# Performance work log

Hardware: AMD Instinct MI355X
Metric: run time of the kernel (lower is better)

## Reference

```python
import jax, jax.numpy as jnp
import numpy as np

N_NODES = 50000
N_EDGES = 800000
HIDDEN = 128


def setup_inputs() -> dict:
    key = jax.random.key(0)
    k_h, k_src, k_dst, k_w1, k_w2 = jax.random.split(key, 5)
    h = jax.random.normal(k_h, (N_NODES, HIDDEN), dtype=jnp.float32)
    src = jax.random.randint(k_src, (N_EDGES,), 0, N_NODES, dtype=jnp.int32)
    dst = jax.random.randint(k_dst, (N_EDGES,), 0, N_NODES, dtype=jnp.int32)
    edge_index = jnp.stack([src, dst], axis=0)
    # MLP params (torch Linear: y = x @ W.T + b); store as [in, out] for einsum
    s1 = 1.0 / np.sqrt(2 * HIDDEN)
    s2 = 1.0 / np.sqrt(HIDDEN)
    W1 = jax.random.uniform(k_w1, (2 * HIDDEN, HIDDEN), jnp.float32, -s1, s1)
    b1 = jnp.zeros((HIDDEN,), jnp.float32)
    W2 = jax.random.uniform(k_w2, (HIDDEN, HIDDEN), jnp.float32, -s2, s2)
    b2 = jnp.zeros((HIDDEN,), jnp.float32)
    return {"h": h, "edge_index": edge_index, "W1": W1, "b1": b1, "W2": W2, "b2": b2}


def reference(h, edge_index, W1, b1, W2, b2):
    src, dst = edge_index[0], edge_index[1]
    n = h.shape[0]
    # scatter-add of gathered source features -> agg [N, H]
    agg = jax.ops.segment_sum(h[src], dst, num_segments=n)
    # degree normalization (clamp_min 1)
    deg = jax.ops.segment_sum(jnp.ones_like(dst, dtype=h.dtype), dst, num_segments=n)
    deg = jnp.maximum(deg, 1.0)[:, None]
    agg = agg / deg
    x = jnp.concatenate([h, agg], axis=1)  # [N, 2H]
    x = jax.nn.relu(x @ W1 + b1)
    x = jax.nn.relu(x @ W2 + b2)
    return x
```

## Files before the change

### kernel.cpp

```cpp
#include <hip/hip_runtime.h>

typedef unsigned short u16;
typedef unsigned int u32;
typedef __attribute__((ext_vector_type(8))) short short8;
typedef __attribute__((ext_vector_type(4))) float f32x4;
typedef __attribute__((ext_vector_type(4))) u32 u32x4;

#define BKT_SHIFT 6
#define BKT_NODES 64
#define CAP 1536
#define EPB 4096
#define NBH 1024

__device__ inline u16 f2bf(float f){ u32 u=__float_as_uint(f); u32 r=((u>>16)&1u)+0x7fffu; return (u16)((u+r)>>16); }

__global__ __launch_bounds__(256) void k_castbin(
    const int* __restrict__ src, const int* __restrict__ dst,
    int* __restrict__ gcnt, u32* __restrict__ recs_g, int nE, int gB,
    const float* __restrict__ h, u16* __restrict__ hbf, int nh8,
    const float* __restrict__ w1, const float* __restrict__ w2,
    u16* __restrict__ w1t, u16* __restrict__ w2t){
  __shared__ u32 rl[EPB];
  __shared__ int hist[NBH];
  __shared__ int curs[NBH];
  int t = threadIdx.x;
  if ((int)blockIdx.x < gB){
    int e0 = blockIdx.x*EPB;
    for (int i=t;i<NBH;i+=256) hist[i]=0;
    __syncthreads();
    #pragma unroll
    for (int i=0;i<EPB/256;i++){
      int e = e0 + i*256 + t;
      u32 rec = 0xffffffffu;
      if (e < nE){
        u32 d = (u32)dst[e];
        u32 s = (u32)src[e];
        u32 bb = d >> BKT_SHIFT;
        rec = (bb<<22) | ((d & (u32)(BKT_NODES-1))<<16) | s;
        atomicAdd(&hist[bb & (NBH-1)], 1);
      }
      rl[i*256+t] = rec;
    }
    __syncthreads();
    for (int i=t;i<NBH;i+=256){
      int c = hist[i];
      curs[i] = c ? atomicAdd(&gcnt[i], c) : 0;
    }
    __syncthreads();
    #pragma unroll
    for (int i=0;i<EPB/256;i++){
      u32 rec = rl[i*256+t];
      if (rec != 0xffffffffu){
        u32 bb = rec>>22;
        int slot = atomicAdd(&curs[bb], 1);
        if (slot < CAP) recs_g[(size_t)bb*CAP + slot] = rec & 0x3fffffu;
      }
    }
  } else {
    int e = ((int)blockIdx.x - gB)*256 + t;
    if (e < nh8){
      float4 a = *(const float4*)(h + (size_t)e*8);
      float4 b = *(const float4*)(h + (size_t)e*8 + 4);
      u32x4 p;
      p.x = (u32)f2bf(a.x) | ((u32)f2bf(a.y)<<16);
      p.y = (u32)f2bf(a.z) | ((u32)f2bf(a.w)<<16);
      p.z = (u32)f2bf(b.x) | ((u32)f2bf(b.y)<<16);
      p.w = (u32)f2bf(b.z) | ((u32)f2bf(b.w)<<16);
      *(u32x4*)(hbf + (size_t)e*8) = p;
    }
    if (e < 256*128){ int k=e>>7, nn=e&127; w1t[nn*256+k]=f2bf(w1[e]); }
    else { int j=e-256*128; if (j<128*128){ int k=j>>7, nn=j&127; w2t[nn*128+k]=f2bf(w2[j]); } }
  }
}

__global__ __launch_bounds__(256, 3) void k_aggmlp(
    const u16* __restrict__ hbf, const u32* __restrict__ recs_g,
    const int* __restrict__ gcnt,
    const u16* __restrict__ w1t, const u16* __restrict__ w2t,
    const float* __restrict__ b1, const float* __restrict__ b2,
    float* __restrict__ out, int n){
  __shared__ __align__(16) u16 xs[64*264];
  __shared__ u32 stage[CAP];
  __shared__ u16 srt[CAP];
  __shared__ int hist[BKT_NODES];
  __shared__ int scn[BKT_NODES];
  __shared__ int cur[BKT_NODES];
  int b = blockIdx.x, t = threadIdx.x;
  int node0 = b*BKT_NODES;

  #pragma unroll
  for (int i=0;i<8;i++){
    int idx = i*256 + t;
    int row = idx>>5, c8 = idx&31;
    int node = node0 + row;
    u32x4 v = {0,0,0,0};
    if (node < n && c8 < 16) v = *(const u32x4*)(hbf + (size_t)node*128 + c8*8);
    *(u32x4*)(&xs[row*264 + c8*8]) = v;
  }

  int cnt = gcnt[b]; if (cnt > CAP) cnt = CAP;
  if (t < BKT_NODES) hist[t] = 0;
  __syncthreads();
  for (int i=t; i<cnt; i+=256){
    u32 r = recs_g[(size_t)b*CAP + i];
    stage[i] = r;
    atomicAdd(&hist[(r>>16)&(BKT_NODES-1)], 1);
  }
  __syncthreads();
  if (t < BKT_NODES) scn[t] = hist[t];
  __syncthreads();
  #pragma unroll
  for (int d=1; d<BKT_NODES; d<<=1){
    int v = 0;
    if (t < BKT_NODES){ v = scn[t]; if (t >= d) v += scn[t-d]; }
    __syncthreads();
    if (t < BKT_NODES) scn[t] = v;
    __syncthreads();
  }
  if (t < BKT_NODES) cur[t] = scn[t] - hist[t];
  __syncthreads();
  for (int i=t; i<cnt; i+=256){
    u32 r = stage[i];
    int slot = atomicAdd(&cur[(r>>16)&(BKT_NODES-1)], 1);
    srt[slot] = (u16)(r & 0xffffu);
  }
  __syncthreads();

  int grp = t>>4, l16g = t&15;
  for (int i=0;i<4;i++){
    int nl = grp*4 + i;
    int node = node0 + nl;
    int deg = 0, st = 0;
    if (node < n){ deg = hist[nl]; st = scn[nl] - deg; }
    float a[8] = {0.f,0.f,0.f,0.f,0.f,0.f,0.f,0.f};
    for (int base=0; base<deg; base+=16){
      int sidx[16];
      #pragma unroll
      for (int j=0;j<16;j++){
        int jj = base + j; if (jj > deg-1) jj = deg-1;
        sidx[j] = srt[st + jj];
      }
      u32x4 vv[16];
      #pragma unroll
      for (int j=0;j<16;j++)
        vv[j] = *(const u32x4*)(hbf + (size_t)sidx[j]*128 + l16g*8);
      #pragma unroll
      for (int j=0;j<16;j++){
        float m = (base+j < deg) ? 1.f : 0.f;
        #pragma unroll
        for (int q=0;q<4;q++){
          u32 u = vv[j][q];
          union{u32 v; float f;} lo,hi; lo.v=u<<16; hi.v=u&0xffff0000u;
          a[q*2]   += m*lo.f;
          a[q*2+1] += m*hi.f;
        }
      }
    }
    if (node < n){
      float inv = 1.f/(float)(deg>0?deg:1);
      u32x4 o;
      o.x = (u32)f2bf(a[0]*inv) | ((u32)f2bf(a[1]*inv)<<16);
      o.y = (u32)f2bf(a[2]*inv) | ((u32)f2bf(a[3]*inv)<<16);
      o.z = (u32)f2bf(a[4]*inv) | ((u32)f2bf(a[5]*inv)<<16);
      o.w = (u32)f2bf(a[6]*inv) | ((u32)f2bf(a[7]*inv)<<16);
      *(u32x4*)(&xs[nl*264 + 128 + l16g*8]) = o;
    }
  }

  int wave=t>>6, lane=t&63, quad=lane>>4, l16=lane&15;
  int nt0 = wave*2;
  const u16* w1p0 = w1t + (size_t)((nt0  )*16 + l16)*256 + quad*8;
  const u16* w1p1 = w1t + (size_t)((nt0+1)*16 + l16)*256 + quad*8;
  short8 wb1[16];
  #pragma unroll
  for (int ks=0;ks<8;ks++){
    wb1[ks*2+0] = *(const short8*)(w1p0 + ks*32);
    wb1[ks*2+1] = *(const short8*)(w1p1 + ks*32);
  }
  __syncthreads();

  f32x4 acc[4][2];
  #pragma unroll
  for (int m=0;m<4;m++){ acc[m][0]=(f32x4){0,0,0,0}; acc[m][1]=(f32x4){0,0,0,0}; }
  #pragma unroll
  for (int ks=0;ks<8;ks++){
    #pragma unroll
    for (int m=0;m<4;m++){
      short8 av = *(const short8*)(&xs[(m*16+l16)*264 + ks*32 + quad*8]);
      acc[m][0] = __builtin_amdgcn_mfma_f32_16x16x32_bf16(av, wb1[ks*2+0], acc[m][0],0,0,0);
      acc[m][1] = __builtin_amdgcn_mfma_f32_16x16x32_bf16(av, wb1[ks*2+1], acc[m][1],0,0,0);
    }
  }

  const u16* w2p0 = w2t + (size_t)((nt0  )*16 + l16)*128 + quad*8;
  const u16* w2p1 = w2t + (size_t)((nt0+1)*16 + l16)*128 + quad*8;
  short8 wb2[8];
  #pragma unroll
  for (int ks=0;ks<4;ks++){
    wb2[ks*2+0] = *(const short8*)(w2p0 + ks*32);
    wb2[ks*2+1] = *(const short8*)(w2p1 + ks*32);
  }
  __syncthreads();

  float bias0 = b1[(nt0  )*16 + l16];
  float bias1 = b1[(nt0+1)*16 + l16];
  #pragma unroll
  for (int m=0;m<4;m++){
    #pragma unroll
    for (int r=0;r<4;r++){
      int row = m*16 + quad*4 + r;
      float v0 = acc[m][0][r] + bias0; v0 = v0>0.f ? v0 : 0.f;
      float v1 = acc[m][1][r] + bias1; v1 = v1>0.f ? v1 : 0.f;
      xs[row*264 + (nt0  )*16 + l16] = f2bf(v0);
      xs[row*264 + (nt0+1)*16 + l16] = f2bf(v1);
    }
  }
  __syncthreads();

  f32x4 acc2[4][2];
  #pragma unroll
  for (int m=0;m<4;m++){ acc2[m][0]=(f32x4){0,0,0,0}; acc2[m][1]=(f32x4){0,0,0,0}; }
  #pragma unroll
  for (int ks=0;ks<4;ks++){
    #pragma unroll
    for (int m=0;m<4;m++){
      short8 av = *(const short8*)(&xs[(m*16+l16)*264 + ks*32 + quad*8]);
      acc2[m][0] = __builtin_amdgcn_mfma_f32_16x16x32_bf16(av, wb2[ks*2+0], acc2[m][0],0,0,0);
      acc2[m][1] = __builtin_amdgcn_mfma_f32_16x16x32_bf16(av, wb2[ks*2+1], acc2[m][1],0,0,0);
    }
  }
  float c0 = b2[(nt0  )*16 + l16];
  float c1 = b2[(nt0+1)*16 + l16];
  #pragma unroll
  for (int m=0;m<4;m++){
    #pragma unroll
    for (int r=0;r<4;r++){
      int node = node0 + m*16 + quad*4 + r;
      if (node<n){
        float v0 = acc2[m][0][r]+c0; v0 = v0>0.f?v0:0.f;
        float v1 = acc2[m][1][r]+c1; v1 = v1>0.f?v1:0.f;
        out[(size_t)node*128 + (nt0  )*16 + l16] = v0;
        out[(size_t)node*128 + (nt0+1)*16 + l16] = v1;
      }
    }
  }
}

extern "C" void kernel_launch(void* const* d_in, const int* in_sizes, int n_in,
                              void* d_out, int out_size, void* d_ws, size_t ws_size,
                              hipStream_t stream){
  const float* h  = (const float*)d_in[0];
  const int*   ei = (const int*)d_in[1];
  const float* W1 = (const float*)d_in[2];
  const float* b1 = (const float*)d_in[3];
  const float* W2 = (const float*)d_in[4];
  const float* b2 = (const float*)d_in[5];
  float* out = (float*)d_out;
  int n  = in_sizes[0] / 128;
  int nE = in_sizes[1] / 2;
  const int* srcI = ei;
  const int* dstI = ei + nE;
  int nbuck = (n + BKT_NODES - 1) >> BKT_SHIFT;

  char* ws = (char*)d_ws;
  u32* recs = (u32*)ws;
  size_t off = (size_t)nbuck*CAP*4;
  int* gcnt = (int*)(ws + off); off += 4096;
  u16* hbf  = (u16*)(ws + off); off += (size_t)n*256;
  off = (off + 15) & ~(size_t)15;
  u16* w1t  = (u16*)(ws + off);
  u16* w2t  = (u16*)(ws + off + 65536);

  hipMemsetAsync(gcnt, 0, NBH*sizeof(int), stream);
  int gB = (nE + EPB - 1)/EPB;
  int nh8 = n*16;
  int castN = nh8 > 49152 ? nh8 : 49152;
  int gC = (castN + 255)/256;
  k_castbin<<<gB+gC, 256, 0, stream>>>(srcI, dstI, gcnt, recs, nE, gB,
                                       h, hbf, nh8, W1, W2, w1t, w2t);
  k_aggmlp<<<nbuck, 256, 0, stream>>>(hbf, recs, gcnt, w1t, w2t, b1, b2, out, n);
}
```

Before: 151.4 us.

## Double block size to 512 threads and split work across eight waves

The fused aggregate+MLP kernel now runs 512 threads per block. Each wave owns one 16-column output tile instead of two, and each 16-lane group aggregates two nodes with 8-edge batches instead of four nodes with 16-edge batches. The LDS stage buffer is dropped, so records are re-read from global memory, and the 64-entry prefix scan uses wave shuffles instead of barrier-separated LDS steps. This is meant to raise parallelism and memory-level concurrency in the gather while cutting barriers and register pressure. In exchange it loads the record list from global memory twice and lowers per-thread gather depth.

```diff
diff --git a/kernel.cpp b/kernel.cpp
--- a/kernel.cpp
+++ b/kernel.cpp
@@ -73,79 +73,74 @@
   }
 }
 
-__global__ __launch_bounds__(256, 3) void k_aggmlp(
+__global__ __launch_bounds__(512, 6) void k_aggmlp(
     const u16* __restrict__ hbf, const u32* __restrict__ recs_g,
     const int* __restrict__ gcnt,
     const u16* __restrict__ w1t, const u16* __restrict__ w2t,
     const float* __restrict__ b1, const float* __restrict__ b2,
     float* __restrict__ out, int n){
   __shared__ __align__(16) u16 xs[64*264];
-  __shared__ u32 stage[CAP];
   __shared__ u16 srt[CAP];
   __shared__ int hist[BKT_NODES];
   __shared__ int scn[BKT_NODES];
   __shared__ int cur[BKT_NODES];
   int b = blockIdx.x, t = threadIdx.x;
   int node0 = b*BKT_NODES;
-
-  #pragma unroll
-  for (int i=0;i<8;i++){
-    int idx = i*256 + t;
+  int cnt = gcnt[b]; if (cnt > CAP) cnt = CAP;
+  const u32* rp = recs_g + (size_t)b*CAP;
+
+  if (t < BKT_NODES) hist[t] = 0;
+  #pragma unroll
+  for (int i=0;i<4;i++){
+    int idx = i*512 + t;
     int row = idx>>5, c8 = idx&31;
     int node = node0 + row;
     u32x4 v = {0,0,0,0};
     if (node < n && c8 < 16) v = *(const u32x4*)(hbf + (size_t)node*128 + c8*8);
     *(u32x4*)(&xs[row*264 + c8*8]) = v;
   }
-
-  int cnt = gcnt[b]; if (cnt > CAP) cnt = CAP;
-  if (t < BKT_NODES) hist[t] = 0;
-  __syncthreads();
-  for (int i=t; i<cnt; i+=256){
-    u32 r = recs_g[(size_t)b*CAP + i];
-    stage[i] = r;
-    atomicAdd(&hist[(r>>16)&(BKT_NODES-1)], 1);
-  }
-  __syncthreads();
-  if (t < BKT_NODES) scn[t] = hist[t];
-  __syncthreads();
-  #pragma unroll
-  for (int d=1; d<BKT_NODES; d<<=1){
-    int v = 0;
-    if (t < BKT_NODES){ v = scn[t]; if (t >= d) v += scn[t-d]; }
-    __syncthreads();
-    if (t < BKT_NODES) scn[t] = v;
-    __syncthreads();
-  }
-  if (t < BKT_NODES) cur[t] = scn[t] - hist[t];
-  __syncthreads();
-  for (int i=t; i<cnt; i+=256){
-    u32 r = stage[i];
+  __syncthreads();
+  for (int i=t; i<cnt; i+=512) atomicAdd(&hist[(rp[i]>>16)&(BKT_NODES-1)], 1);
+  __syncthreads();
+  if (t < BKT_NODES){
+    int v = hist[t];
+    int s = v;
+    #pragma unroll
+    for (int d=1; d<64; d<<=1){
+      int o = __shfl_up(s, d, 64);
+      if (t >= d) s += o;
+    }
+    scn[t] = s;
+    cur[t] = s - v;
+  }
+  __syncthreads();
+  for (int i=t; i<cnt; i+=512){
+    u32 r = rp[i];
     int slot = atomicAdd(&cur[(r>>16)&(BKT_NODES-1)], 1);
     srt[slot] = (u16)(r & 0xffffu);
   }
   __syncthreads();
 
   int grp = t>>4, l16g = t&15;
-  for (int i=0;i<4;i++){
-    int nl = grp*4 + i;
-    int node = node0 + nl;
-    int deg = 0, st = 0;
-    if (node < n){ deg = hist[nl]; st = scn[nl] - deg; }
+  #pragma unroll
+  for (int i=0;i<2;i++){
+    int nl = i*32 + grp;
+    int deg = hist[nl];
+    int st  = scn[nl] - deg;
     float a[8] = {0.f,0.f,0.f,0.f,0.f,0.f,0.f,0.f};
-    for (int base=0; base<deg; base+=16){
-      int sidx[16];
+    for (int base=0; base<deg; base+=8){
+      int sidx[8];
       #pragma unroll
-      for (int j=0;j<16;j++){
+      for (int j=0;j<8;j++){
         int jj = base + j; if (jj > deg-1) jj = deg-1;
         sidx[j] = srt[st + jj];
       }
-      u32x4 vv[16];
+      u32x4 vv[8];
       #pragma unroll
-      for (int j=0;j<16;j++)
+      for (int j=0;j<8;j++)
         vv[j] = *(const u32x4*)(hbf + (size_t)sidx[j]*128 + l16g*8);
       #pragma unroll
-      for (int j=0;j<16;j++){
+      for (int j=0;j<8;j++){
         float m = (base+j < deg) ? 1.f : 0.f;
         #pragma unroll
         for (int q=0;q<4;q++){
@@ -156,91 +151,72 @@
         }
       }
     }
-    if (node < n){
-      float inv = 1.f/(float)(deg>0?deg:1);
-      u32x4 o;
-      o.x = (u32)f2bf(a[0]*inv) | ((u32)f2bf(a[1]*inv)<<16);
-      o.y = (u32)f2bf(a[2]*inv) | ((u32)f2bf(a[3]*inv)<<16);
-      o.z = (u32)f2bf(a[4]*inv) | ((u32)f2bf(a[5]*inv)<<16);
-      o.w = (u32)f2bf(a[6]*inv) | ((u32)f2bf(a[7]*inv)<<16);
-      *(u32x4*)(&xs[nl*264 + 128 + l16g*8]) = o;
-    }
+    float inv = 1.f/(float)(deg>0?deg:1);
+    u32x4 o;
+    o.x = (u32)f2bf(a[0]*inv) | ((u32)f2bf(a[1]*inv)<<16);
+    o.y = (u32)f2bf(a[2]*inv) | ((u32)f2bf(a[3]*inv)<<16);
+    o.z = (u32)f2bf(a[4]*inv) | ((u32)f2bf(a[5]*inv)<<16);
+    o.w = (u32)f2bf(a[6]*inv) | ((u32)f2bf(a[7]*inv)<<16);
+    *(u32x4*)(&xs[nl*264 + 128 + l16g*8]) = o;
   }
 
   int wave=t>>6, lane=t&63, quad=lane>>4, l16=lane&15;
-  int nt0 = wave*2;
-  const u16* w1p0 = w1t + (size_t)((nt0  )*16 + l16)*256 + quad*8;
-  const u16* w1p1 = w1t + (size_t)((nt0+1)*16 + l16)*256 + quad*8;
-  short8 wb1[16];
-  #pragma unroll
-  for (int ks=0;ks<8;ks++){
-    wb1[ks*2+0] = *(const short8*)(w1p0 + ks*32);
-    wb1[ks*2+1] = *(const short8*)(w1p1 + ks*32);
-  }
-  __syncthreads();
-
-  f32x4 acc[4][2];
-  #pragma unroll
-  for (int m=0;m<4;m++){ acc[m][0]=(f32x4){0,0,0,0}; acc[m][1]=(f32x4){0,0,0,0}; }
+  const u16* w1p = w1t + (size_t)(wave*16 + l16)*256 + quad*8;
+  short8 wb1[8];
+  #pragma unroll
+  for (int ks=0;ks<8;ks++) wb1[ks] = *(const short8*)(w1p + ks*32);
+  __syncthreads();
+
+  f32x4 acc[4];
+  #pragma unroll
+  for (int m=0;m<4;m++) acc[m]=(f32x4){0,0,0,0};
   #pragma unroll
   for (int ks=0;ks<8;ks++){
     #pragma unroll
     for (int m=0;m<4;m++){
       short8 av = *(const short8*)(&xs[(m*16+l16)*264 + ks*32 + quad*8]);
-      acc[m][0] = __builtin_amdgcn_mfma_f32_16x16x32_bf16(av, wb1[ks*2+0], acc[m][0],0,0,0);
-      acc[m][1] = __builtin_amdgcn_mfma_f32_16x16x32_bf16(av, wb1[ks*2+1], acc[m][1],0,0,0);
-    }
-  }
-
-  const u16* w2p0 = w2t + (size_t)((nt0  )*16 + l16)*128 + quad*8;
-  const u16* w2p1 = w2t + (size_t)((nt0+1)*16 + l16)*128 + quad*8;
-  short8 wb2[8];
-  #pragma unroll
-  for (int ks=0;ks<4;ks++){
-    wb2[ks*2+0] = *(const short8*)(w2p0 + ks*32);
-    wb2[ks*2+1] = *(const short8*)(w2p1 + ks*32);
-  }
-  __syncthreads();
-
-  float bias0 = b1[(nt0  )*16 + l16];
-  float bias1 = b1[(nt0+1)*16 + l16];
+      acc[m] = __builtin_amdgcn_mfma_f32_16x16x32_bf16(av, wb1[ks], acc[m],0,0,0);
+    }
+  }
+
+  const u16* w2p = w2t + (size_t)(wave*16 + l16)*128 + quad*8;
+  short8 wb2[4];
+  #pragma unroll
+  for (int ks=0;ks<4;ks++) wb2[ks] = *(const short8*)(w2p + ks*32);
+  __syncthreads();
+
+  float bias = b1[wave*16 + l16];
   #pragma unroll
   for (int m=0;m<4;m++){
     #pragma unroll
     for (int r=0;r<4;r++){
       int row = m*16 + quad*4 + r;
-      float v0 = acc[m][0][r] + bias0; v0 = v0>0.f ? v0 : 0.f;
-      float v1 = acc[m][1][r] + bias1; v1 = v1>0.f ? v1 : 0.f;
-      xs[row*264 + (nt0  )*16 + l16] = f2bf(v0);
-      xs[row*264 + (nt0+1)*16 + l16] = f2bf(v1);
-    }
-  }
-  __syncthreads();
-
-  f32x4 acc2[4][2];
-  #pragma unroll
-  for (int m=0;m<4;m++){ acc2[m][0]=(f32x4){0,0,0,0}; acc2[m][1]=(f32x4){0,0,0,0}; }
+      float v0 = acc[m][r] + bias; v0 = v0>0.f ? v0 : 0.f;
+      xs[row*264 + wave*16 + l16] = f2bf(v0);
+    }
+  }
+  __syncthreads();
+
+  f32x4 acc2[4];
+  #pragma unroll
+  for (int m=0;m<4;m++) acc2[m]=(f32x4){0,0,0,0};
   #pragma unroll
   for (int ks=0;ks<4;ks++){
     #pragma unroll
     for (int m=0;m<4;m++){
       short8 av = *(const short8*)(&xs[(m*16+l16)*264 + ks*32 + quad*8]);
-      acc2[m][0] = __builtin_amdgcn_mfma_f32_16x16x32_bf16(av, wb2[ks*2+0], acc2[m][0],0,0,0);
-      acc2[m][1] = __builtin_amdgcn_mfma_f32_16x16x32_bf16(av, wb2[ks*2+1], acc2[m][1],0,0,0);
-    }
-  }
-  float c0 = b2[(nt0  )*16 + l16];
-  float c1 = b2[(nt0+1)*16 + l16];
+      acc2[m] = __builtin_amdgcn_mfma_f32_16x16x32_bf16(av, wb2[ks], acc2[m],0,0,0);
+    }
+  }
+  float c0 = b2[wave*16 + l16];
   #pragma unroll
   for (int m=0;m<4;m++){
     #pragma unroll
     for (int r=0;r<4;r++){
       int node = node0 + m*16 + quad*4 + r;
       if (node<n){
-        float v0 = acc2[m][0][r]+c0; v0 = v0>0.f?v0:0.f;
-        float v1 = acc2[m][1][r]+c1; v1 = v1>0.f?v1:0.f;
-        out[(size_t)node*128 + (nt0  )*16 + l16] = v0;
-        out[(size_t)node*128 + (nt0+1)*16 + l16] = v1;
+        float v0 = acc2[m][r]+c0; v0 = v0>0.f?v0:0.f;
+        out[(size_t)node*128 + wave*16 + l16] = v0;
       }
     }
   }
@@ -278,5 +254,5 @@
   int gC = (castN + 255)/256;
   k_castbin<<<gB+gC, 256, 0, stream>>>(srcI, dstI, gcnt, recs, nE, gB,
                                        h, hbf, nh8, W1, W2, w1t, w2t);
-  k_aggmlp<<<nbuck, 256, 0, stream>>>(hbf, recs, gcnt, w1t, w2t, b1, b2, out, n);
+  k_aggmlp<<<nbuck, 512, 0, stream>>>(hbf, recs, gcnt, w1t, w2t, b1, b2, out, n);
 }
```

Measured after the change: 148.5 us. About the same (-1.9%).

## Fuse pipeline into one persistent cooperative kernel with grid-wide syncs

Applied to the files above, without the earlier changes.

Replaces the two-kernel pipeline (cast/bin, then aggregate+MLP) with a single cooperative persistent kernel that has four phases separated by grid.sync. Binning uses smaller 1024-edge chunks. Per-bucket sorting now writes sorted source lists and node offsets to global memory. Aggregation is redone as one wave per node that writes bf16 results into scratch space in the output buffer, and the MLP phase reads them back. This removes a launch and the memset and spreads aggregation evenly across all waves, at the cost of grid-wide barriers and extra global round-trips for the sorted indices and aggregated features.

```diff
diff --git a/kernel.cpp b/kernel.cpp
--- a/kernel.cpp
+++ b/kernel.cpp
@@ -1,4 +1,7 @@
 #include <hip/hip_runtime.h>
+#include <hip/hip_cooperative_groups.h>
+
+namespace cg = cooperative_groups;
 
 typedef unsigned short u16;
 typedef unsigned int u32;
@@ -9,239 +12,250 @@
 #define BKT_SHIFT 6
 #define BKT_NODES 64
 #define CAP 1536
-#define EPB 4096
 #define NBH 1024
 
 __device__ inline u16 f2bf(float f){ u32 u=__float_as_uint(f); u32 r=((u>>16)&1u)+0x7fffu; return (u16)((u+r)>>16); }
 
-__global__ __launch_bounds__(256) void k_castbin(
-    const int* __restrict__ src, const int* __restrict__ dst,
-    int* __restrict__ gcnt, u32* __restrict__ recs_g, int nE, int gB,
-    const float* __restrict__ h, u16* __restrict__ hbf, int nh8,
+__global__ __launch_bounds__(256, 3) void k_all(
+    const float* __restrict__ h, const int* __restrict__ src, const int* __restrict__ dst,
     const float* __restrict__ w1, const float* __restrict__ w2,
-    u16* __restrict__ w1t, u16* __restrict__ w2t){
-  __shared__ u32 rl[EPB];
-  __shared__ int hist[NBH];
-  __shared__ int curs[NBH];
+    const float* __restrict__ b1, const float* __restrict__ b2,
+    u16* __restrict__ hbf, u32* __restrict__ recs, int* __restrict__ gcnt,
+    u16* __restrict__ srt_g, u32* __restrict__ nd_g,
+    u16* __restrict__ w1t, u16* __restrict__ w2t,
+    float* __restrict__ out, int n, int nE, int nbuck){
+  cg::grid_group grid = cg::this_grid();
+  __shared__ __align__(16) char smem[64*264*2];
+
   int t = threadIdx.x;
-  if ((int)blockIdx.x < gB){
-    int e0 = blockIdx.x*EPB;
-    for (int i=t;i<NBH;i+=256) hist[i]=0;
-    __syncthreads();
-    #pragma unroll
-    for (int i=0;i<EPB/256;i++){
-      int e = e0 + i*256 + t;
-      u32 rec = 0xffffffffu;
-      if (e < nE){
-        u32 d = (u32)dst[e];
-        u32 s = (u32)src[e];
-        u32 bb = d >> BKT_SHIFT;
-        rec = (bb<<22) | ((d & (u32)(BKT_NODES-1))<<16) | s;
-        atomicAdd(&hist[bb & (NBH-1)], 1);
-      }
-      rl[i*256+t] = rec;
+  int gt = blockIdx.x*256 + t;
+  int GT = gridDim.x*256;
+  u32* outw = (u32*)out;
+  const u32* hbfw = (const u32*)hbf;
+
+  int nh8 = n*16;
+  for (int e=gt; e<nh8; e+=GT){
+    float4 a = *(const float4*)(h + (size_t)e*8);
+    float4 b = *(const float4*)(h + (size_t)e*8 + 4);
+    u32x4 p;
+    p.x = (u32)f2bf(a.x) | ((u32)f2bf(a.y)<<16);
+    p.y = (u32)f2bf(a.z) | ((u32)f2bf(a.w)<<16);
+    p.z = (u32)f2bf(b.x) | ((u32)f2bf(b.y)<<16);
+    p.w = (u32)f2bf(b.z) | ((u32)f2bf(b.w)<<16);
+    *(u32x4*)(hbf + (size_t)e*8) = p;
+  }
+  for (int e=gt; e<256*128; e+=GT){ int k=e>>7, nn=e&127; w1t[nn*256+k]=f2bf(w1[e]); }
+  for (int e=gt; e<128*128; e+=GT){ int k=e>>7, nn=e&127; w2t[nn*128+k]=f2bf(w2[e]); }
+  for (int i=gt; i<NBH; i+=GT) gcnt[i]=0;
+  grid.sync();
+
+  {
+    u32* rl   = (u32*)smem;
+    int* hist = (int*)(smem + 4096);
+    int* curs = (int*)(smem + 8192);
+    int nchunk = (nE + 1023) >> 10;
+    for (int c = blockIdx.x; c < nchunk; c += gridDim.x){
+      int e0 = c<<10;
+      for (int i=t;i<NBH;i+=256) hist[i]=0;
+      __syncthreads();
+      #pragma unroll
+      for (int i=0;i<4;i++){
+        int e = e0 + i*256 + t;
+        u32 rec = 0xffffffffu;
+        if (e < nE){
+          u32 d=(u32)dst[e], s=(u32)src[e];
+          u32 bb = d>>BKT_SHIFT;
+          rec = (bb<<22) | ((d & (u32)(BKT_NODES-1))<<16) | s;
+          atomicAdd(&hist[bb], 1);
+        }
+        rl[i*256+t] = rec;
+      }
+      __syncthreads();
+      for (int i=t;i<NBH;i+=256){
+        int cc = hist[i];
+        curs[i] = cc ? atomicAdd(&gcnt[i], cc) : 0;
+      }
+      __syncthreads();
+      #pragma unroll
+      for (int i=0;i<4;i++){
+        u32 rec = rl[i*256+t];
+        if (rec != 0xffffffffu){
+          u32 bb = rec>>22;
+          int slot = atomicAdd(&curs[bb], 1);
+          if (slot < CAP) recs[(size_t)bb*CAP + slot] = rec & 0x3fffffu;
+        }
+      }
+      __syncthreads();
     }
-    __syncthreads();
-    for (int i=t;i<NBH;i+=256){
-      int c = hist[i];
-      curs[i] = c ? atomicAdd(&gcnt[i], c) : 0;
+  }
+  grid.sync();
+
+  {
+    u32* stg  = (u32*)smem;
+    u16* srt  = (u16*)(smem + 6144);
+    int* shist= (int*)(smem + 9216);
+    int* sscn = (int*)(smem + 9472);
+    int* scur = (int*)(smem + 9728);
+    for (int b = blockIdx.x; b < nbuck; b += gridDim.x){
+      int cnt = gcnt[b]; if (cnt > CAP) cnt = CAP;
+      const u32* rp = recs + (size_t)b*CAP;
+      if (t < BKT_NODES) shist[t] = 0;
+      __syncthreads();
+      for (int i=t; i<cnt; i+=256){
+        u32 r = rp[i];
+        stg[i] = r;
+        atomicAdd(&shist[(r>>16)&(BKT_NODES-1)], 1);
+      }
+      __syncthreads();
+      if (t < BKT_NODES){
+        int v = shist[t]; int s = v;
+        #pragma unroll
+        for (int d=1; d<64; d<<=1){ int o=__shfl_up(s,d,64); if (t>=d) s+=o; }
+        sscn[t]=s; scur[t]=s-v;
+      }
+      __syncthreads();
+      for (int i=t; i<cnt; i+=256){
+        u32 r = stg[i];
+        int slot = atomicAdd(&scur[(r>>16)&(BKT_NODES-1)],1);
+        srt[slot] = (u16)(r & 0xffffu);
+      }
+      __syncthreads();
+      u32* gw2 = (u32*)(srt_g + (size_t)b*CAP);
+      const u32* sw = (const u32*)srt;
+      int cw = (cnt+1)>>1;
+      for (int i=t;i<cw;i+=256) gw2[i]=sw[i];
+      if (t < BKT_NODES){
+        int node = b*BKT_NODES + t;
+        if (node<n) nd_g[node] = (u32)(sscn[t]-shist[t]) | ((u32)shist[t]<<16);
+      }
+      __syncthreads();
     }
-    __syncthreads();
-    #pragma unroll
-    for (int i=0;i<EPB/256;i++){
-      u32 rec = rl[i*256+t];
-      if (rec != 0xffffffffu){
-        u32 bb = rec>>22;
-        int slot = atomicAdd(&curs[bb], 1);
-        if (slot < CAP) recs_g[(size_t)bb*CAP + slot] = rec & 0x3fffffu;
-      }
+  }
+  grid.sync();
+
+  {
+    int gw = gt>>6;
+    int NW = GT>>6;
+    int lane = t & 63;
+    for (int node=gw; node<n; node+=NW){
+      u32 nd = nd_g[node];
+      int st=(int)(nd&0xffffu), deg=(int)(nd>>16);
+      const u16* sp = srt_g + (size_t)(node>>6)*CAP + st;
+      float a0=0.f, a1=0.f;
+      for (int base=0;base<deg;base+=16){
+        int sidx[16];
+        #pragma unroll
+        for (int j=0;j<16;j++){ int jj=base+j; if (jj>deg-1) jj=deg-1; sidx[j]=sp[jj]; }
+        u32 vv[16];
+        #pragma unroll
+        for (int j=0;j<16;j++) vv[j] = hbfw[(size_t)sidx[j]*64 + lane];
+        #pragma unroll
+        for (int j=0;j<16;j++){
+          float m = (base+j<deg)?1.f:0.f;
+          union{u32 u; float f;} lo,hi; lo.u=vv[j]<<16; hi.u=vv[j]&0xffff0000u;
+          a0+=m*lo.f; a1+=m*hi.f;
+        }
+      }
+      float inv = 1.f/(float)(deg>0?deg:1);
+      outw[(size_t)node*128 + 64 + lane] = (u32)f2bf(a0*inv)|((u32)f2bf(a1*inv)<<16);
     }
-  } else {
-    int e = ((int)blockIdx.x - gB)*256 + t;
-    if (e < nh8){
-      float4 a = *(const float4*)(h + (size_t)e*8);
-      float4 b = *(const float4*)(h + (size_t)e*8 + 4);
-      u32x4 p;
-      p.x = (u32)f2bf(a.x) | ((u32)f2bf(a.y)<<16);
-      p.y = (u32)f2bf(a.z) | ((u32)f2bf(a.w)<<16);
-      p.z = (u32)f2bf(b.x) | ((u32)f2bf(b.y)<<16);
-      p.w = (u32)f2bf(b.z) | ((u32)f2bf(b.w)<<16);
-      *(u32x4*)(hbf + (size_t)e*8) = p;
-    }
-    if (e < 256*128){ int k=e>>7, nn=e&127; w1t[nn*256+k]=f2bf(w1[e]); }
-    else { int j=e-256*128; if (j<128*128){ int k=j>>7, nn=j&127; w2t[nn*128+k]=f2bf(w2[j]); } }
-  }
-}
-
-__global__ __launch_bounds__(256, 3) void k_aggmlp(
-    const u16* __restrict__ hbf, const u32* __restrict__ recs_g,
-    const int* __restrict__ gcnt,
-    const u16* __restrict__ w1t, const u16* __restrict__ w2t,
-    const float* __restrict__ b1, const float* __restrict__ b2,
-    float* __restrict__ out, int n){
-  __shared__ __align__(16) u16 xs[64*264];
-  __shared__ u32 stage[CAP];
-  __shared__ u16 srt[CAP];
-  __shared__ int hist[BKT_NODES];
-  __shared__ int scn[BKT_NODES];
-  __shared__ int cur[BKT_NODES];
-  int b = blockIdx.x, t = threadIdx.x;
-  int node0 = b*BKT_NODES;
-
-  #pragma unroll
-  for (int i=0;i<8;i++){
-    int idx = i*256 + t;
-    int row = idx>>5, c8 = idx&31;
-    int node = node0 + row;
-    u32x4 v = {0,0,0,0};
-    if (node < n && c8 < 16) v = *(const u32x4*)(hbf + (size_t)node*128 + c8*8);
-    *(u32x4*)(&xs[row*264 + c8*8]) = v;
-  }
-
-  int cnt = gcnt[b]; if (cnt > CAP) cnt = CAP;
-  if (t < BKT_NODES) hist[t] = 0;
-  __syncthreads();
-  for (int i=t; i<cnt; i+=256){
-    u32 r = recs_g[(size_t)b*CAP + i];
-    stage[i] = r;
-    atomicAdd(&hist[(r>>16)&(BKT_NODES-1)], 1);
-  }
-  __syncthreads();
-  if (t < BKT_NODES) scn[t] = hist[t];
-  __syncthreads();
-  #pragma unroll
-  for (int d=1; d<BKT_NODES; d<<=1){
-    int v = 0;
-    if (t < BKT_NODES){ v = scn[t]; if (t >= d) v += scn[t-d]; }
-    __syncthreads();
-    if (t < BKT_NODES) scn[t] = v;
-    __syncthreads();
-  }
-  if (t < BKT_NODES) cur[t] = scn[t] - hist[t];
-  __syncthreads();
-  for (int i=t; i<cnt; i+=256){
-    u32 r = stage[i];
-    int slot = atomicAdd(&cur[(r>>16)&(BKT_NODES-1)], 1);
-    srt[slot] = (u16)(r & 0xffffu);
-  }
-  __syncthreads();
-
-  int grp = t>>4, l16g = t&15;
-  for (int i=0;i<4;i++){
-    int nl = grp*4 + i;
-    int node = node0 + nl;
-    int deg = 0, st = 0;
-    if (node < n){ deg = hist[nl]; st = scn[nl] - deg; }
-    float a[8] = {0.f,0.f,0.f,0.f,0.f,0.f,0.f,0.f};
-    for (int base=0; base<deg; base+=16){
-      int sidx[16];
-      #pragma unroll
-      for (int j=0;j<16;j++){
-        int jj = base + j; if (jj > deg-1) jj = deg-1;
-        sidx[j] = srt[st + jj];
-      }
-      u32x4 vv[16];
-      #pragma unroll
-      for (int j=0;j<16;j++)
-        vv[j] = *(const u32x4*)(hbf + (size_t)sidx[j]*128 + l16g*8);
-      #pragma unroll
-      for (int j=0;j<16;j++){
-        float m = (base+j < deg) ? 1.f : 0.f;
-        #pragma unroll
-        for (int q=0;q<4;q++){
-          u32 u = vv[j][q];
-          union{u32 v; float f;} lo,hi; lo.v=u<<16; hi.v=u&0xffff0000u;
-          a[q*2]   += m*lo.f;
-          a[q*2+1] += m*hi.f;
-        }
-      }
-    }
-    if (node < n){
-      float inv = 1.f/(float)(deg>0?deg:1);
-      u32x4 o;
-      o.x = (u32)f2bf(a[0]*inv) | ((u32)f2bf(a[1]*inv)<<16);
-      o.y = (u32)f2bf(a[2]*inv) | ((u32)f2bf(a[3]*inv)<<16);
-      o.z = (u32)f2bf(a[4]*inv) | ((u32)f2bf(a[5]*inv)<<16);
-      o.w = (u32)f2bf(a[6]*inv) | ((u32)f2bf(a[7]*inv)<<16);
-      *(u32x4*)(&xs[nl*264 + 128 + l16g*8]) = o;
-    }
-  }
-
-  int wave=t>>6, lane=t&63, quad=lane>>4, l16=lane&15;
-  int nt0 = wave*2;
-  const u16* w1p0 = w1t + (size_t)((nt0  )*16 + l16)*256 + quad*8;
-  const u16* w1p1 = w1t + (size_t)((nt0+1)*16 + l16)*256 + quad*8;
-  short8 wb1[16];
-  #pragma unroll
-  for (int ks=0;ks<8;ks++){
-    wb1[ks*2+0] = *(const short8*)(w1p0 + ks*32);
-    wb1[ks*2+1] = *(const short8*)(w1p1 + ks*32);
-  }
-  __syncthreads();
-
-  f32x4 acc[4][2];
-  #pragma unroll
-  for (int m=0;m<4;m++){ acc[m][0]=(f32x4){0,0,0,0}; acc[m][1]=(f32x4){0,0,0,0}; }
-  #pragma unroll
-  for (int ks=0;ks<8;ks++){
-    #pragma unroll
-    for (int m=0;m<4;m++){
-      short8 av = *(const short8*)(&xs[(m*16+l16)*264 + ks*32 + quad*8]);
-      acc[m][0] = __builtin_amdgcn_mfma_f32_16x16x32_bf16(av, wb1[ks*2+0], acc[m][0],0,0,0);
-      acc[m][1] = __builtin_amdgcn_mfma_f32_16x16x32_bf16(av, wb1[ks*2+1], acc[m][1],0,0,0);
-    }
-  }
-
-  const u16* w2p0 = w2t + (size_t)((nt0  )*16 + l16)*128 + quad*8;
-  const u16* w2p1 = w2t + (size_t)((nt0+1)*16 + l16)*128 + quad*8;
-  short8 wb2[8];
-  #pragma unroll
-  for (int ks=0;ks<4;ks++){
-    wb2[ks*2+0] = *(const short8*)(w2p0 + ks*32);
-    wb2[ks*2+1] = *(const short8*)(w2p1 + ks*32);
-  }
-  __syncthreads();
-
-  float bias0 = b1[(nt0  )*16 + l16];
-  float bias1 = b1[(nt0+1)*16 + l16];
-  #pragma unroll
-  for (int m=0;m<4;m++){
-    #pragma unroll
-    for (int r=0;r<4;r++){
-      int row = m*16 + quad*4 + r;
-      float v0 = acc[m][0][r] + bias0; v0 = v0>0.f ? v0 : 0.f;
-      float v1 = acc[m][1][r] + bias1; v1 = v1>0.f ? v1 : 0.f;
-      xs[row*264 + (nt0  )*16 + l16] = f2bf(v0);
-      xs[row*264 + (nt0+1)*16 + l16] = f2bf(v1);
-    }
-  }
-  __syncthreads();
-
-  f32x4 acc2[4][2];
-  #pragma unroll
-  for (int m=0;m<4;m++){ acc2[m][0]=(f32x4){0,0,0,0}; acc2[m][1]=(f32x4){0,0,0,0}; }
-  #pragma unroll
-  for (int ks=0;ks<4;ks++){
-    #pragma unroll
-    for (int m=0;m<4;m++){
-      short8 av = *(const short8*)(&xs[(m*16+l16)*264 + ks*32 + quad*8]);
-      acc2[m][0] = __builtin_amdgcn_mfma_f32_16x16x32_bf16(av, wb2[ks*2+0], acc2[m][0],0,0,0);
-      acc2[m][1] = __builtin_amdgcn_mfma_f32_16x16x32_bf16(av, wb2[ks*2+1], acc2[m][1],0,0,0);
-    }
-  }
-  float c0 = b2[(nt0  )*16 + l16];
-  float c1 = b2[(nt0+1)*16 + l16];
-  #pragma unroll
-  for (int m=0;m<4;m++){
-    #pragma unroll
-    for (int r=0;r<4;r++){
-      int node = node0 + m*16 + quad*4 + r;
-      if (node<n){
-        float v0 = acc2[m][0][r]+c0; v0 = v0>0.f?v0:0.f;
-        float v1 = acc2[m][1][r]+c1; v1 = v1>0.f?v1:0.f;
-        out[(size_t)node*128 + (nt0  )*16 + l16] = v0;
-        out[(size_t)node*128 + (nt0+1)*16 + l16] = v1;
-      }
+  }
+  grid.sync();
+
+  {
+    u16* xs = (u16*)smem;
+    int wave=t>>6, lane=t&63, quad=lane>>4, l16=lane&15;
+    int nt0 = wave*2;
+    for (int tile = blockIdx.x; tile < nbuck; tile += gridDim.x){
+      int node0 = tile*BKT_NODES;
+      #pragma unroll
+      for (int i=0;i<8;i++){
+        int idx = i*256 + t;
+        int row = idx>>5, c8 = idx&31;
+        int node = node0 + row;
+        u32x4 v = {0,0,0,0};
+        if (node < n){
+          if (c8 < 16) v = *(const u32x4*)(hbf + (size_t)node*128 + c8*8);
+          else         v = *(const u32x4*)(outw + (size_t)node*128 + 64 + (c8-16)*4);
+        }
+        *(u32x4*)(&xs[row*264 + c8*8]) = v;
+      }
+      const u16* w1p0 = w1t + (size_t)((nt0  )*16 + l16)*256 + quad*8;
+      const u16* w1p1 = w1t + (size_t)((nt0+1)*16 + l16)*256 + quad*8;
+      short8 wb1[16];
+      #pragma unroll
+      for (int ks=0;ks<8;ks++){
+        wb1[ks*2+0] = *(const short8*)(w1p0 + ks*32);
+        wb1[ks*2+1] = *(const short8*)(w1p1 + ks*32);
+      }
+      __syncthreads();
+
+      f32x4 acc[4][2];
+      #pragma unroll
+      for (int m=0;m<4;m++){ acc[m][0]=(f32x4){0,0,0,0}; acc[m][1]=(f32x4){0,0,0,0}; }
+      #pragma unroll
+      for (int ks=0;ks<8;ks++){
+        #pragma unroll
+        for (int m=0;m<4;m++){
+          short8 av = *(const short8*)(&xs[(m*16+l16)*264 + ks*32 + quad*8]);
+          acc[m][0] = __builtin_amdgcn_mfma_f32_16x16x32_bf16(av, wb1[ks*2+0], acc[m][0],0,0,0);
+          acc[m][1] = __builtin_amdgcn_mfma_f32_16x16x32_bf16(av, wb1[ks*2+1], acc[m][1],0,0,0);
+        }
+      }
+
+      const u16* w2p0 = w2t + (size_t)((nt0  )*16 + l16)*128 + quad*8;
+      const u16* w2p1 = w2t + (size_t)((nt0+1)*16 + l16)*128 + quad*8;
+      short8 wb2[8];
+      #pragma unroll
+      for (int ks=0;ks<4;ks++){
+        wb2[ks*2+0] = *(const short8*)(w2p0 + ks*32);
+        wb2[ks*2+1] = *(const short8*)(w2p1 + ks*32);
+      }
+      __syncthreads();
+
+      float bias0 = b1[(nt0  )*16 + l16];
+      float bias1 = b1[(nt0+1)*16 + l16];
+      #pragma unroll
+      for (int m=0;m<4;m++){
+        #pragma unroll
+        for (int r=0;r<4;r++){
+          int row = m*16 + quad*4 + r;
+          float v0 = acc[m][0][r] + bias0; v0 = v0>0.f ? v0 : 0.f;
+          float v1 = acc[m][1][r] + bias1; v1 = v1>0.f ? v1 : 0.f;
+          xs[row*264 + (nt0  )*16 + l16] = f2bf(v0);
+          xs[row*264 + (nt0+1)*16 + l16] = f2bf(v1);
+        }
+      }
+      __syncthreads();
+
+      f32x4 acc2[4][2];
+      #pragma unroll
+      for (int m=0;m<4;m++){ acc2[m][0]=(f32x4){0,0,0,0}; acc2[m][1]=(f32x4){0,0,0,0}; }
+      #pragma unroll
+      for (int ks=0;ks<4;ks++){
+        #pragma unroll
+        for (int m=0;m<4;m++){
+          short8 av = *(const short8*)(&xs[(m*16+l16)*264 + ks*32 + quad*8]);
+          acc2[m][0] = __builtin_amdgcn_mfma_f32_16x16x32_bf16(av, wb2[ks*2+0], acc2[m][0],0,0,0);
+          acc2[m][1] = __builtin_amdgcn_mfma_f32_16x16x32_bf16(av, wb2[ks*2+1], acc2[m][1],0,0,0);
+        }
+      }
+      float c0 = b2[(nt0  )*16 + l16];
+      float c1 = b2[(nt0+1)*16 + l16];
+      #pragma unroll
+      for (int m=0;m<4;m++){
+        #pragma unroll
+        for (int r=0;r<4;r++){
+          int node = node0 + m*16 + quad*4 + r;
+          if (node<n){
+            float v0 = acc2[m][0][r]+c0; v0 = v0>0.f?v0:0.f;
+            float v1 = acc2[m][1][r]+c1; v1 = v1>0.f?v1:0.f;
+            out[(size_t)node*128 + (nt0  )*16 + l16] = v0;
+            out[(size_t)node*128 + (nt0+1)*16 + l16] = v1;
+          }
+        }
+      }
+      __syncthreads();
     }
   }
 }
@@ -268,15 +282,29 @@
   int* gcnt = (int*)(ws + off); off += 4096;
   u16* hbf  = (u16*)(ws + off); off += (size_t)n*256;
   off = (off + 15) & ~(size_t)15;
+  u16* srt_g = (u16*)(ws + off); off += (size_t)nbuck*CAP*2;
+  off = (off + 15) & ~(size_t)15;
+  u32* nd_g = (u32*)(ws + off); off += (size_t)((n+63)&~63)*4;
+  off = (off + 15) & ~(size_t)15;
   u16* w1t  = (u16*)(ws + off);
   u16* w2t  = (u16*)(ws + off + 65536);
 
-  hipMemsetAsync(gcnt, 0, NBH*sizeof(int), stream);
-  int gB = (nE + EPB - 1)/EPB;
-  int nh8 = n*16;
-  int castN = nh8 > 49152 ? nh8 : 49152;
-  int gC = (castN + 255)/256;
-  k_castbin<<<gB+gC, 256, 0, stream>>>(srcI, dstI, gcnt, recs, nE, gB,
-                                       h, hbf, nh8, W1, W2, w1t, w2t);
-  k_aggmlp<<<nbuck, 256, 0, stream>>>(hbf, recs, gcnt, w1t, w2t, b1, b2, out, n);
+  static int gridBlocks = 0;
+  if (gridBlocks == 0){
+    int nb = 0;
+    hipOccupancyMaxActiveBlocksPerMultiprocessor(&nb, k_all, 256, 0);
+    if (nb < 1) nb = 1;
+    int dev = 0; hipGetDevice(&dev);
+    hipDeviceProp_t prop;
+    hipGetDeviceProperties(&prop, dev);
+    int ncu = prop.multiProcessorCount > 0 ? prop.multiProcessorCount : 256;
+    gridBlocks = nb * ncu;
+    if (gridBlocks > 2048) gridBlocks = 2048;
+  }
+
+  void* args[] = { (void*)&h, (void*)&srcI, (void*)&dstI, (void*)&W1, (void*)&W2,
+                   (void*)&b1, (void*)&b2, (void*)&hbf, (void*)&recs, (void*)&gcnt,
+                   (void*)&srt_g, (void*)&nd_g, (void*)&w1t, (void*)&w2t, (void*)&out,
+                   (void*)&n, (void*)&nE, (void*)&nbuck };
+  hipLaunchCooperativeKernel((void*)k_all, dim3(gridBlocks), dim3(256), args, 0, stream);
 }
```

Result: slower. 367.4 us (+142.7%).
